# Kernel optimization log

Hardware: AMD Instinct MI355X
Metric: run time of the kernel (lower is better)

Reference implementation:

```python
import jax, jax.numpy as jnp
import numpy as np

NUM_TAGS = 64
SOS_IDX, EOS_IDX, PAD_IDX = 1, 2, 0
NEG = -10000.0


def _make_trans(key):
    t = np.array(jax.random.normal(key, (NUM_TAGS, NUM_TAGS), dtype=jnp.float32))
    t[SOS_IDX, :] = NEG
    t[:, EOS_IDX] = NEG
    t[:, PAD_IDX] = NEG
    t[PAD_IDX, :] = NEG
    t[PAD_IDX, EOS_IDX] = 0.0
    t[PAD_IDX, PAD_IDX] = 0.0
    return jnp.asarray(t)


def setup_inputs() -> dict:
    key = jax.random.key(0)
    k_h, k_len, k_tr = jax.random.split(key, 3)
    B, T = 256, 1024
    h = jax.random.normal(k_h, (B, T, NUM_TAGS), dtype=jnp.float32)
    # variable-length prefix mask (1.0 for valid steps)
    lengths = jax.random.randint(k_len, (B,), 1, T + 1)
    mask = (jnp.arange(T)[None, :] < lengths[:, None]).astype(jnp.float32)
    trans = _make_trans(k_tr)
    return {"h": h, "mask": mask, "trans": trans}


def reference(h, mask, trans):
    # h: [B, T, N] emissions; mask: [B, T]; trans: [N_next, N_prev]
    B, T, N = h.shape
    init = jnp.full((B, N), NEG, dtype=h.dtype).at[:, SOS_IDX].set(0.0)

    def step(score, xs):
        h_t, m_t = xs  # [B, N], [B]
        # score[b, prev] + emit[b, next] + trans[next, prev] -> lse over prev
        s = score[:, None, :] + h_t[:, :, None] + trans[None, :, :]
        new = jax.nn.logsumexp(s, axis=-1)  # [B, N]
        m = m_t[:, None]
        score = new * m + score * (1.0 - m)
        return score, None

    score, _ = jax.lax.scan(step, init, (jnp.swapaxes(h, 0, 1), mask.T))
    # terminal transition to EOS, then partition function per batch element
    return jax.nn.logsumexp(score + trans[EOS_IDX][None, :], axis=-1)  # [B]
```

## Files before the change

kernel.cpp:

```cpp
#include <hip/hip_runtime.h>

#define BATCH 256
#define TT 1024
#define NN 64
#define CHUNK 64
#define NCH (TT / CHUNK)
#define SOS 1
#define EOSI 2
#define LN2F 0.6931471805599453f
#define LOG2E 1.4426950408889634f

typedef short bf16x8 __attribute__((ext_vector_type(8)));
typedef float f32x4 __attribute__((ext_vector_type(4)));

__device__ __forceinline__ unsigned short f2bf(float x) {
  unsigned u = __float_as_uint(x);
  u += 0x7fffu + ((u >> 16) & 1u);
  return (unsigned short)(u >> 16);
}
__device__ __forceinline__ float bf2f(unsigned short v) { return __uint_as_float(((unsigned)v) << 16); }

__device__ __forceinline__ unsigned cvtpk(float lo, float hi) {
  unsigned r;
  asm("v_cvt_pk_bf16_f32 %0, %1, %2" : "=v"(r) : "v"(lo), "v"(hi));
  return r;
}

__device__ __forceinline__ int tadr(int k, int c) {
  return ((c >> 4) << 11) + ((k >> 5) << 10) + (((k >> 3) & 3) << 8) + ((c & 15) << 4) + ((k & 7) << 1);
}

__device__ __forceinline__ int wave_len(const float* mask, int b, int l) {
  float ls = 0.f;
#pragma unroll
  for (int c = 0; c < 4; ++c) {
    float4 m4 = *reinterpret_cast<const float4*>(mask + (size_t)b * TT + c * 256 + l * 4);
    ls += (m4.x + m4.y) + (m4.z + m4.w);
  }
#pragma unroll
  for (int m = 1; m < 64; m <<= 1) ls += __shfl_xor(ls, m, 64);
  return (int)(ls + 0.5f);
}

__global__ __launch_bounds__(64, 4) void crf_chunk(const float* __restrict__ h,
                                                   const float* __restrict__ mask,
                                                   const float* __restrict__ trans,
                                                   unsigned short* __restrict__ mats,
                                                   float* __restrict__ scales) {
  __shared__ char R[8192 + 256];
  float* ehs = (float*)(R + 8192);
  const int l = threadIdx.x;
  const int b = blockIdx.x & (BATCH - 1);
  const int c = blockIdx.x >> 8;

  const int len = wave_len(mask, b, l);
  const int t0 = c * CHUNK;
  if (t0 >= len) return;
  const int nstep = min(CHUNK, len - t0);

  bf16x8 ef[4][2];
#pragma unroll
  for (int I = 0; I < 4; ++I)
#pragma unroll
    for (int Kc = 0; Kc < 2; ++Kc) {
      const int row = 16 * I + (l & 15);
      const int k0 = 32 * Kc + 8 * (l >> 4);
      const float* p = trans + row * 64 + k0;
      bf16x8 v;
#pragma unroll
      for (int e = 0; e < 8; ++e) v[e] = (short)f2bf(__expf(p[e]));
      ef[I][Kc] = v;
    }

#pragma unroll
  for (int i = 0; i < 8; ++i) *(f32x4*)(R + ((i * 64 + l) << 4)) = f32x4{0.f, 0.f, 0.f, 0.f};
  *(unsigned short*)(R + tadr(l, l)) = 0x3F80;
  asm volatile("s_waitcnt lgkmcnt(0)" ::: "memory");

  int eA = 0, eB = 0, esum = 0;
  float hv = h[((size_t)b * TT + t0) * NN + l];

  for (int t = 0; t < nstep; ++t) {
    const int tn = (t + 1 < nstep) ? t + 1 : t;
    float hv_next = h[((size_t)b * TT + t0 + tn) * NN + l];
    ehs[l] = exp2f(fmaf(hv, LOG2E, (float)(-eA)));
    esum += eA;

    float mloc = 0.f;
#pragma unroll
    for (int J = 0; J < 4; ++J) {
      bf16x8 f0 = *(bf16x8*)(R + ((2 * J) << 10) + (l << 4));
      bf16x8 f1 = *(bf16x8*)(R + ((2 * J + 1) << 10) + (l << 4));
      f32x4 a[4];
#pragma unroll
      for (int I = 0; I < 4; ++I) a[I] = f32x4{0.f, 0.f, 0.f, 0.f};
#pragma unroll
      for (int I = 0; I < 4; ++I) {
        a[I] = __builtin_amdgcn_mfma_f32_16x16x32_bf16(ef[I][0], f0, a[I], 0, 0, 0);
        a[I] = __builtin_amdgcn_mfma_f32_16x16x32_bf16(ef[I][1], f1, a[I], 0, 0, 0);
      }
#pragma unroll
      for (int I = 0; I < 4; ++I) {
        f32x4 s4 = *(f32x4*)(ehs + 16 * I + 4 * (l >> 4));
        f32x4 v = a[I] * s4;
        mloc = fmaxf(mloc, fmaxf(fmaxf(v[0], v[1]), fmaxf(v[2], v[3])));
        const int r0 = 16 * I + 4 * (l >> 4);
        const int cc = 16 * J + (l & 15);
        *(uint2*)(R + tadr(r0, cc)) = uint2{cvtpk(v[0], v[1]), cvtpk(v[2], v[3])};
      }
    }
#pragma unroll
    for (int m = 1; m < 64; m <<= 1) mloc = fmaxf(mloc, __shfl_xor(mloc, m, 64));
    const int eNew = (__float_as_int(mloc) >> 23) - 127;
    eA = eB;
    eB = eNew;
    hv = hv_next;
    asm volatile("s_waitcnt lgkmcnt(0)" ::: "memory");
  }

  const float scF = __int_as_float((127 - eB) << 23);
  esum += eB;
  unsigned short* gm = mats + (size_t)(b * NCH + c) * 4096;
#pragma unroll
  for (int j0 = 0; j0 < 64; j0 += 8) {
    unsigned q[4];
#pragma unroll
    for (int p = 0; p < 4; ++p) {
      float x0 = bf2f(*(unsigned short*)(R + tadr(l, j0 + 2 * p))) * scF;
      float x1 = bf2f(*(unsigned short*)(R + tadr(l, j0 + 2 * p + 1))) * scF;
      q[p] = cvtpk(x0, x1);
    }
    *(uint4*)(gm + l * 64 + j0) = uint4{q[0], q[1], q[2], q[3]};
  }
  if (l == 0) scales[b * NCH + c] = LN2F * (float)esum;
}

__global__ __launch_bounds__(64) void crf_fold(const float* __restrict__ mask,
                                               const float* __restrict__ trans,
                                               const unsigned short* __restrict__ mats,
                                               const float* __restrict__ scales,
                                               float* __restrict__ out) {
  __shared__ float pv[NN];
  const int l = threadIdx.x;
  const int b = blockIdx.x;
  const int len = wave_len(mask, b, l);
  const int nc = (len + CHUNK - 1) / CHUNK;

  float stot = (l < nc) ? scales[b * NCH + l] : 0.f;
#pragma unroll
  for (int m = 1; m < 64; m <<= 1) stot += __shfl_xor(stot, m, 64);

  pv[l] = (l == SOS) ? 1.f : 0.f;
  asm volatile("s_waitcnt lgkmcnt(0)" ::: "memory");

  int eA = 0, esum = 0;
  for (int c = 0; c < nc; ++c) {
    const uint4* Mr = (const uint4*)(mats + (size_t)(b * NCH + c) * 4096 + l * 64);
    uint4 U[8];
#pragma unroll
    for (int j = 0; j < 8; ++j) U[j] = Mr[j];
    const float sc = __int_as_float((127 - eA) << 23);
    esum += eA;
    float ac0 = 0.f, ac1 = 0.f, ac2 = 0.f, ac3 = 0.f;
#pragma unroll
    for (int j = 0; j < 8; ++j) {
      f32x4 pa = *(f32x4*)(pv + j * 8);
      f32x4 pb = *(f32x4*)(pv + j * 8 + 4);
      uint4 q = U[j];
      ac0 = fmaf(__uint_as_float(q.x << 16), pa[0], ac0);
      ac1 = fmaf(__uint_as_float(q.x & 0xffff0000u), pa[1], ac1);
      ac2 = fmaf(__uint_as_float(q.y << 16), pa[2], ac2);
      ac3 = fmaf(__uint_as_float(q.y & 0xffff0000u), pa[3], ac3);
      ac0 = fmaf(__uint_as_float(q.z << 16), pb[0], ac0);
      ac1 = fmaf(__uint_as_float(q.z & 0xffff0000u), pb[1], ac1);
      ac2 = fmaf(__uint_as_float(q.w << 16), pb[2], ac2);
      ac3 = fmaf(__uint_as_float(q.w & 0xffff0000u), pb[3], ac3);
    }
    float pn = ((ac0 + ac1) + (ac2 + ac3)) * sc;
    float mm = pn;
#pragma unroll
    for (int m = 1; m < 64; m <<= 1) mm = fmaxf(mm, __shfl_xor(mm, m, 64));
    eA = (__float_as_int(mm) >> 23) - 127;
    pv[l] = pn;
    asm volatile("s_waitcnt lgkmcnt(0)" ::: "memory");
  }

  float s = pv[l] * __expf(trans[EOSI * NN + l]);
#pragma unroll
  for (int m = 1; m < 64; m <<= 1) s += __shfl_xor(s, m, 64);
  if (l == 0) out[b] = __logf(s) + LN2F * (float)esum + stot;
}

extern "C" void kernel_launch(void* const* d_in, const int* in_sizes, int n_in,
                              void* d_out, int out_size, void* d_ws, size_t ws_size,
                              hipStream_t stream) {
  const float* h = (const float*)d_in[0];
  const float* mask = (const float*)d_in[1];
  const float* trans = (const float*)d_in[2];
  float* out = (float*)d_out;

  unsigned short* mats = (unsigned short*)d_ws;
  float* scales = (float*)((char*)d_ws + (size_t)BATCH * NCH * 4096 * 2);

  hipLaunchKernelGGL(crf_chunk, dim3(BATCH * NCH), dim3(64), 0, stream, h, mask, trans, mats, scales);
  hipLaunchKernelGGL(crf_fold, dim3(BATCH), dim3(64), 0, stream, mask, trans, mats, scales, out);
}
```

Before: 179.2 us.

## Replace per-step wave max reduction with lagged single-lane exponent proxy

The per-step 64-lane shuffle max reduction that picks the rescaling exponent is replaced by one readlane of a proxy maximum. The proxy is taken from a subset of accumulator entries and applied only every other step, which removes a serial cross-lane dependency from the recurrence. The change also prefetches the next LDS B-fragments during the MFMA loop, uses packed f32 multiplies, loads emission scales once per step, remaps blocks to be batch-major, and lowers the occupancy hint. The risk is numerical: a single-entry proxy with a lagged rescale could let values drift toward bf16 overflow or underflow for atypical inputs.

```diff
diff --git a/kernel.cpp b/kernel.cpp
--- a/kernel.cpp
+++ b/kernel.cpp
@@ -12,6 +12,7 @@
 
 typedef short bf16x8 __attribute__((ext_vector_type(8)));
 typedef float f32x4 __attribute__((ext_vector_type(4)));
+typedef float f32x2 __attribute__((ext_vector_type(2)));
 
 __device__ __forceinline__ unsigned short f2bf(float x) {
   unsigned u = __float_as_uint(x);
@@ -25,6 +26,11 @@
   asm("v_cvt_pk_bf16_f32 %0, %1, %2" : "=v"(r) : "v"(lo), "v"(hi));
   return r;
 }
+__device__ __forceinline__ f32x2 pkmul(f32x2 a, f32x2 b) {
+  f32x2 r;
+  asm("v_pk_mul_f32 %0, %1, %2" : "=v"(r) : "v"(a), "v"(b));
+  return r;
+}
 
 __device__ __forceinline__ int tadr(int k, int c) {
   return ((c >> 4) << 11) + ((k >> 5) << 10) + (((k >> 3) & 3) << 8) + ((c & 15) << 4) + ((k & 7) << 1);
@@ -42,7 +48,7 @@
   return (int)(ls + 0.5f);
 }
 
-__global__ __launch_bounds__(64, 4) void crf_chunk(const float* __restrict__ h,
+__global__ __launch_bounds__(64, 3) void crf_chunk(const float* __restrict__ h,
                                                    const float* __restrict__ mask,
                                                    const float* __restrict__ trans,
                                                    unsigned short* __restrict__ mats,
@@ -50,8 +56,9 @@
   __shared__ char R[8192 + 256];
   float* ehs = (float*)(R + 8192);
   const int l = threadIdx.x;
-  const int b = blockIdx.x & (BATCH - 1);
-  const int c = blockIdx.x >> 8;
+  const int h4 = l >> 4;
+  const int b = blockIdx.x >> 4;
+  const int c = blockIdx.x & (NCH - 1);
 
   const int len = wave_len(mask, b, l);
   const int t0 = c * CHUNK;
@@ -64,8 +71,7 @@
 #pragma unroll
     for (int Kc = 0; Kc < 2; ++Kc) {
       const int row = 16 * I + (l & 15);
-      const int k0 = 32 * Kc + 8 * (l >> 4);
-      const float* p = trans + row * 64 + k0;
+      const float* p = trans + row * 64 + 32 * Kc + 8 * h4;
       bf16x8 v;
 #pragma unroll
       for (int e = 0; e < 8; ++e) v[e] = (short)f2bf(__expf(p[e]));
@@ -77,49 +83,65 @@
   *(unsigned short*)(R + tadr(l, l)) = 0x3F80;
   asm volatile("s_waitcnt lgkmcnt(0)" ::: "memory");
 
-  int eA = 0, eB = 0, esum = 0;
-  float hv = h[((size_t)b * TT + t0) * NN + l];
+  int ePend = 0;
+  int esum = 0;
+  const float* hp = h + ((size_t)b * TT + t0) * NN + l;
+  float hv = *hp;
+  hp += NN;
 
   for (int t = 0; t < nstep; ++t) {
-    const int tn = (t + 1 < nstep) ? t + 1 : t;
-    float hv_next = h[((size_t)b * TT + t0 + tn) * NN + l];
-    ehs[l] = exp2f(fmaf(hv, LOG2E, (float)(-eA)));
-    esum += eA;
-
-    float mloc = 0.f;
+    float hv_next = hv;
+    if (t + 1 < nstep) hv_next = *hp;
+    hp += NN;
+
+    const int ec = ((t & 1) == 0) ? ePend : 0;
+    esum += ec;
+    ehs[l] = exp2f(fmaf(hv, LOG2E, (float)(-ec)));
+    f32x4 eh4[4];
+#pragma unroll
+    for (int I = 0; I < 4; ++I) eh4[I] = *(f32x4*)(ehs + 16 * I + 4 * h4);
+
+    bf16x8 fc0 = *(bf16x8*)(R + 0 + (l << 4));
+    bf16x8 fc1 = *(bf16x8*)(R + 1024 + (l << 4));
+    float prox = 0.f;
 #pragma unroll
     for (int J = 0; J < 4; ++J) {
-      bf16x8 f0 = *(bf16x8*)(R + ((2 * J) << 10) + (l << 4));
-      bf16x8 f1 = *(bf16x8*)(R + ((2 * J + 1) << 10) + (l << 4));
+      bf16x8 fn0, fn1;
+      if (J < 3) {
+        fn0 = *(bf16x8*)(R + (2 * J + 2) * 1024 + (l << 4));
+        fn1 = *(bf16x8*)(R + (2 * J + 3) * 1024 + (l << 4));
+      }
       f32x4 a[4];
 #pragma unroll
       for (int I = 0; I < 4; ++I) a[I] = f32x4{0.f, 0.f, 0.f, 0.f};
 #pragma unroll
       for (int I = 0; I < 4; ++I) {
-        a[I] = __builtin_amdgcn_mfma_f32_16x16x32_bf16(ef[I][0], f0, a[I], 0, 0, 0);
-        a[I] = __builtin_amdgcn_mfma_f32_16x16x32_bf16(ef[I][1], f1, a[I], 0, 0, 0);
+        a[I] = __builtin_amdgcn_mfma_f32_16x16x32_bf16(ef[I][0], fc0, a[I], 0, 0, 0);
+        a[I] = __builtin_amdgcn_mfma_f32_16x16x32_bf16(ef[I][1], fc1, a[I], 0, 0, 0);
       }
 #pragma unroll
       for (int I = 0; I < 4; ++I) {
-        f32x4 s4 = *(f32x4*)(ehs + 16 * I + 4 * (l >> 4));
-        f32x4 v = a[I] * s4;
-        mloc = fmaxf(mloc, fmaxf(fmaxf(v[0], v[1]), fmaxf(v[2], v[3])));
-        const int r0 = 16 * I + 4 * (l >> 4);
+        f32x2 vlo = pkmul(f32x2{a[I][0], a[I][1]}, f32x2{eh4[I][0], eh4[I][1]});
+        f32x2 vhi = pkmul(f32x2{a[I][2], a[I][3]}, f32x2{eh4[I][2], eh4[I][3]});
+        if (J == 0 && (I == 1 || I == 2))
+          prox = fmaxf(prox, fmaxf(fmaxf(vlo[0], vlo[1]), fmaxf(vhi[0], vhi[1])));
+        const int r0 = 16 * I + 4 * h4;
         const int cc = 16 * J + (l & 15);
-        *(uint2*)(R + tadr(r0, cc)) = uint2{cvtpk(v[0], v[1]), cvtpk(v[2], v[3])};
+        *(uint2*)(R + tadr(r0, cc)) = uint2{cvtpk(vlo[0], vlo[1]), cvtpk(vhi[0], vhi[1])};
       }
-    }
-#pragma unroll
-    for (int m = 1; m < 64; m <<= 1) mloc = fmaxf(mloc, __shfl_xor(mloc, m, 64));
-    const int eNew = (__float_as_int(mloc) >> 23) - 127;
-    eA = eB;
-    eB = eNew;
+      fc0 = fn0;
+      fc1 = fn1;
+    }
+    if ((t & 1) == 0) {
+      float px = __int_as_float(__builtin_amdgcn_readlane(__float_as_int(prox), 5));
+      ePend = (__float_as_int(px) >> 23) - 127;
+    }
     hv = hv_next;
     asm volatile("s_waitcnt lgkmcnt(0)" ::: "memory");
   }
 
-  const float scF = __int_as_float((127 - eB) << 23);
-  esum += eB;
+  const float scF = __int_as_float((127 - ePend) << 23);
+  esum += ePend;
   unsigned short* gm = mats + (size_t)(b * NCH + c) * 4096;
 #pragma unroll
   for (int j0 = 0; j0 < 64; j0 += 8) {
```

New measurement: 146.0 us. -18.5%, faster.

## Split chunk transfer matrix across four waves with per-wave column slices and scales

Applied to the files above, without the earlier changes.

The chunk kernel now uses 256-thread blocks where each of four waves propagates a 16-column slice of the 64x64 chunk transfer matrix independently. This cuts each wave's per-step MFMA and LDS work by a factor of four and shortens the serial dependency chain. The emission exponentials are double-buffered and prefetched two steps ahead. The per-step max reduction shrinks to a partial shuffle plus readlane. Each wave keeps its own exponent, so the fold kernel rescales each 16-column group of the carried vector by the per-wave exponent differences. The cost is extra scale bookkeeping and a little more fold work, and the coarser rescaling carries some risk of range or precision loss.

```diff
diff --git a/kernel.cpp b/kernel.cpp
--- a/kernel.cpp
+++ b/kernel.cpp
@@ -4,7 +4,7 @@
 #define TT 1024
 #define NN 64
 #define CHUNK 64
-#define NCH (TT / CHUNK)
+#define NCH 16
 #define SOS 1
 #define EOSI 2
 #define LN2F 0.6931471805599453f
@@ -19,15 +19,14 @@
   return (unsigned short)(u >> 16);
 }
 __device__ __forceinline__ float bf2f(unsigned short v) { return __uint_as_float(((unsigned)v) << 16); }
-
 __device__ __forceinline__ unsigned cvtpk(float lo, float hi) {
   unsigned r;
   asm("v_cvt_pk_bf16_f32 %0, %1, %2" : "=v"(r) : "v"(lo), "v"(hi));
   return r;
 }
 
-__device__ __forceinline__ int tadr(int k, int c) {
-  return ((c >> 4) << 11) + ((k >> 5) << 10) + (((k >> 3) & 3) << 8) + ((c & 15) << 4) + ((k & 7) << 1);
+__device__ __forceinline__ int padr(int k, int c) {
+  return ((k >> 5) << 10) + (((k >> 3) & 3) << 8) + (c << 4) + ((k & 7) << 1);
 }
 
 __device__ __forceinline__ int wave_len(const float* mask, int b, int l) {
@@ -42,14 +41,21 @@
   return (int)(ls + 0.5f);
 }
 
-__global__ __launch_bounds__(64, 4) void crf_chunk(const float* __restrict__ h,
-                                                   const float* __restrict__ mask,
-                                                   const float* __restrict__ trans,
-                                                   unsigned short* __restrict__ mats,
-                                                   float* __restrict__ scales) {
-  __shared__ char R[8192 + 256];
-  float* ehs = (float*)(R + 8192);
-  const int l = threadIdx.x;
+__global__ __launch_bounds__(256, 4) void crf_chunk(const float* __restrict__ h,
+                                                    const float* __restrict__ mask,
+                                                    const float* __restrict__ trans,
+                                                    unsigned short* __restrict__ mats,
+                                                    int* __restrict__ scalesI) {
+  __shared__ char lds[4 * 2048 + 4 * 512];
+  const int tid = threadIdx.x;
+  const int w = tid >> 6;
+  const int l = tid & 63;
+  const int h4 = l >> 4;
+  const int cl = l & 15;
+  char* P = lds + w * 2048;
+  float* ehs0 = (float*)(lds + 8192 + w * 512);
+  float* ehs1 = ehs0 + 64;
+
   const int b = blockIdx.x & (BATCH - 1);
   const int c = blockIdx.x >> 8;
 
@@ -63,9 +69,7 @@
   for (int I = 0; I < 4; ++I)
 #pragma unroll
     for (int Kc = 0; Kc < 2; ++Kc) {
-      const int row = 16 * I + (l & 15);
-      const int k0 = 32 * Kc + 8 * (l >> 4);
-      const float* p = trans + row * 64 + k0;
+      const float* p = trans + (16 * I + cl) * 64 + 32 * Kc + 8 * h4;
       bf16x8 v;
 #pragma unroll
       for (int e = 0; e < 8; ++e) v[e] = (short)f2bf(__expf(p[e]));
@@ -73,72 +77,73 @@
     }
 
 #pragma unroll
-  for (int i = 0; i < 8; ++i) *(f32x4*)(R + ((i * 64 + l) << 4)) = f32x4{0.f, 0.f, 0.f, 0.f};
-  *(unsigned short*)(R + tadr(l, l)) = 0x3F80;
-  asm volatile("s_waitcnt lgkmcnt(0)" ::: "memory");
-
-  int eA = 0, eB = 0, esum = 0;
-  float hv = h[((size_t)b * TT + t0) * NN + l];
+  for (int i = 0; i < 2; ++i) *(f32x4*)(P + ((i * 64 + l) << 4)) = f32x4{0.f, 0.f, 0.f, 0.f};
+  if (l < 16) *(unsigned short*)(P + padr(16 * w + l, l)) = 0x3F80;
+
+  const float* hb = h + ((size_t)b * TT + t0) * NN + l;
+  ehs0[l] = exp2f(hb[0] * LOG2E);
+  asm volatile("" ::: "memory");
+
+  float hvN = hb[(size_t)min(1, nstep - 1) * NN];
+  float hvN2 = hb[(size_t)min(2, nstep - 1) * NN];
+  int esum = 0, ecCur = 0, eM1 = 0;
 
   for (int t = 0; t < nstep; ++t) {
-    const int tn = (t + 1 < nstep) ? t + 1 : t;
-    float hv_next = h[((size_t)b * TT + t0 + tn) * NN + l];
-    ehs[l] = exp2f(fmaf(hv, LOG2E, (float)(-eA)));
-    esum += eA;
-
-    float mloc = 0.f;
-#pragma unroll
-    for (int J = 0; J < 4; ++J) {
-      bf16x8 f0 = *(bf16x8*)(R + ((2 * J) << 10) + (l << 4));
-      bf16x8 f1 = *(bf16x8*)(R + ((2 * J + 1) << 10) + (l << 4));
-      f32x4 a[4];
-#pragma unroll
-      for (int I = 0; I < 4; ++I) a[I] = f32x4{0.f, 0.f, 0.f, 0.f};
-#pragma unroll
-      for (int I = 0; I < 4; ++I) {
-        a[I] = __builtin_amdgcn_mfma_f32_16x16x32_bf16(ef[I][0], f0, a[I], 0, 0, 0);
-        a[I] = __builtin_amdgcn_mfma_f32_16x16x32_bf16(ef[I][1], f1, a[I], 0, 0, 0);
-      }
-#pragma unroll
-      for (int I = 0; I < 4; ++I) {
-        f32x4 s4 = *(f32x4*)(ehs + 16 * I + 4 * (l >> 4));
-        f32x4 v = a[I] * s4;
-        mloc = fmaxf(mloc, fmaxf(fmaxf(v[0], v[1]), fmaxf(v[2], v[3])));
-        const int r0 = 16 * I + 4 * (l >> 4);
-        const int cc = 16 * J + (l & 15);
-        *(uint2*)(R + tadr(r0, cc)) = uint2{cvtpk(v[0], v[1]), cvtpk(v[2], v[3])};
-      }
-    }
-#pragma unroll
-    for (int m = 1; m < 64; m <<= 1) mloc = fmaxf(mloc, __shfl_xor(mloc, m, 64));
-    const int eNew = (__float_as_int(mloc) >> 23) - 127;
-    eA = eB;
-    eB = eNew;
-    hv = hv_next;
-    asm volatile("s_waitcnt lgkmcnt(0)" ::: "memory");
-  }
-
-  const float scF = __int_as_float((127 - eB) << 23);
-  esum += eB;
-  unsigned short* gm = mats + (size_t)(b * NCH + c) * 4096;
-#pragma unroll
-  for (int j0 = 0; j0 < 64; j0 += 8) {
-    unsigned q[4];
-#pragma unroll
-    for (int p = 0; p < 4; ++p) {
-      float x0 = bf2f(*(unsigned short*)(R + tadr(l, j0 + 2 * p))) * scF;
-      float x1 = bf2f(*(unsigned short*)(R + tadr(l, j0 + 2 * p + 1))) * scF;
-      q[p] = cvtpk(x0, x1);
-    }
-    *(uint4*)(gm + l * 64 + j0) = uint4{q[0], q[1], q[2], q[3]};
-  }
-  if (l == 0) scales[b * NCH + c] = LN2F * (float)esum;
+    esum += ecCur;
+    float* ehsW = ((t + 1) & 1) ? ehs1 : ehs0;
+    ehsW[l] = exp2f(fmaf(hvN, LOG2E, -(float)eM1));
+    ecCur = eM1;
+    hvN = hvN2;
+    hvN2 = hb[(size_t)min(t + 3, nstep - 1) * NN];
+
+    float* ehsR = (t & 1) ? ehs1 : ehs0;
+    bf16x8 fc0 = *(bf16x8*)(P + (l << 4));
+    bf16x8 fc1 = *(bf16x8*)(P + 1024 + (l << 4));
+    f32x4 eh4[4];
+#pragma unroll
+    for (int I = 0; I < 4; ++I) eh4[I] = *(f32x4*)(ehsR + 16 * I + 4 * h4);
+
+    f32x4 a[4];
+#pragma unroll
+    for (int I = 0; I < 4; ++I) a[I] = f32x4{0.f, 0.f, 0.f, 0.f};
+#pragma unroll
+    for (int I = 0; I < 4; ++I) {
+      a[I] = __builtin_amdgcn_mfma_f32_16x16x32_bf16(ef[I][0], fc0, a[I], 0, 0, 0);
+      a[I] = __builtin_amdgcn_mfma_f32_16x16x32_bf16(ef[I][1], fc1, a[I], 0, 0, 0);
+    }
+    float prox = 0.f;
+#pragma unroll
+    for (int I = 0; I < 4; ++I) {
+      f32x4 v = a[I] * eh4[I];
+      prox = fmaxf(prox, fmaxf(fmaxf(v[0], v[1]), fmaxf(v[2], v[3])));
+      *(uint2*)(P + padr(16 * I + 4 * h4, cl)) = uint2{cvtpk(v[0], v[1]), cvtpk(v[2], v[3])};
+    }
+    prox = fmaxf(prox, __shfl_xor(prox, 16, 64));
+    prox = fmaxf(prox, __shfl_xor(prox, 32, 64));
+    float px = __int_as_float(__builtin_amdgcn_readlane(__float_as_int(prox), 5));
+    eM1 = (__float_as_int(px) >> 23) - 127;
+    asm volatile("" ::: "memory");
+  }
+
+  const float scF = __int_as_float((127 - eM1) << 23);
+  esum += eM1;
+  unsigned short* gm = mats + (size_t)(b * NCH + c) * 4096 + l * 64 + 16 * w;
+  unsigned q[8];
+#pragma unroll
+  for (int p = 0; p < 8; ++p) {
+    float x0 = bf2f(*(unsigned short*)(P + padr(l, 2 * p))) * scF;
+    float x1 = bf2f(*(unsigned short*)(P + padr(l, 2 * p + 1))) * scF;
+    q[p] = cvtpk(x0, x1);
+  }
+  *(uint4*)gm = uint4{q[0], q[1], q[2], q[3]};
+  *(uint4*)(gm + 8) = uint4{q[4], q[5], q[6], q[7]};
+  if (l == 0) scalesI[(b * NCH + c) * 4 + w] = esum;
 }
 
 __global__ __launch_bounds__(64) void crf_fold(const float* __restrict__ mask,
                                                const float* __restrict__ trans,
                                                const unsigned short* __restrict__ mats,
-                                               const float* __restrict__ scales,
+                                               const int* __restrict__ scalesI,
                                                float* __restrict__ out) {
   __shared__ float pv[NN];
   const int l = threadIdx.x;
@@ -146,49 +151,52 @@
   const int len = wave_len(mask, b, l);
   const int nc = (len + CHUNK - 1) / CHUNK;
 
-  float stot = (l < nc) ? scales[b * NCH + l] : 0.f;
-#pragma unroll
-  for (int m = 1; m < 64; m <<= 1) stot += __shfl_xor(stot, m, 64);
-
-  pv[l] = (l == SOS) ? 1.f : 0.f;
-  asm volatile("s_waitcnt lgkmcnt(0)" ::: "memory");
-
-  int eA = 0, esum = 0;
+  float pr = (l == SOS) ? 1.f : 0.f;
+  int eA = 0;
+  long esumT = 0;
+
   for (int c = 0; c < nc; ++c) {
+    const int* sI = scalesI + (b * NCH + c) * 4;
+    const int e0 = sI[0], e1 = sI[1], e2 = sI[2], e3 = sI[3];
+    const int S = max(max(e0, e1), max(e2, e3));
+    const int g = l >> 4;
+    int dl = (g == 0) ? e0 : (g == 1) ? e1 : (g == 2) ? e2 : e3;
+    dl -= S;
+    pv[l] = ldexpf(pr, dl - eA);
+    asm volatile("" ::: "memory");
+    esumT += S + eA;
+
     const uint4* Mr = (const uint4*)(mats + (size_t)(b * NCH + c) * 4096 + l * 64);
     uint4 U[8];
 #pragma unroll
     for (int j = 0; j < 8; ++j) U[j] = Mr[j];
-    const float sc = __int_as_float((127 - eA) << 23);
-    esum += eA;
     float ac0 = 0.f, ac1 = 0.f, ac2 = 0.f, ac3 = 0.f;
 #pragma unroll
     for (int j = 0; j < 8; ++j) {
       f32x4 pa = *(f32x4*)(pv + j * 8);
       f32x4 pb = *(f32x4*)(pv + j * 8 + 4);
-      uint4 q = U[j];
-      ac0 = fmaf(__uint_as_float(q.x << 16), pa[0], ac0);
-      ac1 = fmaf(__uint_as_float(q.x & 0xffff0000u), pa[1], ac1);
-      ac2 = fmaf(__uint_as_float(q.y << 16), pa[2], ac2);
-      ac3 = fmaf(__uint_as_float(q.y & 0xffff0000u), pa[3], ac3);
-      ac0 = fmaf(__uint_as_float(q.z << 16), pb[0], ac0);
-      ac1 = fmaf(__uint_as_float(q.z & 0xffff0000u), pb[1], ac1);
-      ac2 = fmaf(__uint_as_float(q.w << 16), pb[2], ac2);
-      ac3 = fmaf(__uint_as_float(q.w & 0xffff0000u), pb[3], ac3);
-    }
-    float pn = ((ac0 + ac1) + (ac2 + ac3)) * sc;
-    float mm = pn;
+      uint4 qq = U[j];
+      ac0 = fmaf(__uint_as_float(qq.x << 16), pa[0], ac0);
+      ac1 = fmaf(__uint_as_float(qq.x & 0xffff0000u), pa[1], ac1);
+      ac2 = fmaf(__uint_as_float(qq.y << 16), pa[2], ac2);
+      ac3 = fmaf(__uint_as_float(qq.y & 0xffff0000u), pa[3], ac3);
+      ac0 = fmaf(__uint_as_float(qq.z << 16), pb[0], ac0);
+      ac1 = fmaf(__uint_as_float(qq.z & 0xffff0000u), pb[1], ac1);
+      ac2 = fmaf(__uint_as_float(qq.w << 16), pb[2], ac2);
+      ac3 = fmaf(__uint_as_float(qq.w & 0xffff0000u), pb[3], ac3);
+    }
+    pr = (ac0 + ac1) + (ac2 + ac3);
+    float mm = pr;
 #pragma unroll
     for (int m = 1; m < 64; m <<= 1) mm = fmaxf(mm, __shfl_xor(mm, m, 64));
     eA = (__float_as_int(mm) >> 23) - 127;
-    pv[l] = pn;
-    asm volatile("s_waitcnt lgkmcnt(0)" ::: "memory");
-  }
-
-  float s = pv[l] * __expf(trans[EOSI * NN + l]);
+    asm volatile("" ::: "memory");
+  }
+
+  float s = pr * __expf(trans[EOSI * NN + l]);
 #pragma unroll
   for (int m = 1; m < 64; m <<= 1) s += __shfl_xor(s, m, 64);
-  if (l == 0) out[b] = __logf(s) + LN2F * (float)esum + stot;
+  if (l == 0) out[b] = __logf(s) + LN2F * (float)esumT;
 }
 
 extern "C" void kernel_launch(void* const* d_in, const int* in_sizes, int n_in,
@@ -200,8 +208,8 @@
   float* out = (float*)d_out;
 
   unsigned short* mats = (unsigned short*)d_ws;
-  float* scales = (float*)((char*)d_ws + (size_t)BATCH * NCH * 4096 * 2);
-
-  hipLaunchKernelGGL(crf_chunk, dim3(BATCH * NCH), dim3(64), 0, stream, h, mask, trans, mats, scales);
-  hipLaunchKernelGGL(crf_fold, dim3(BATCH), dim3(64), 0, stream, mask, trans, mats, scales, out);
-}
+  int* scalesI = (int*)((char*)d_ws + (size_t)BATCH * NCH * 4096 * 2);
+
+  hipLaunchKernelGGL(crf_chunk, dim3(BATCH * NCH), dim3(256), 0, stream, h, mask, trans, mats, scalesI);
+  hipLaunchKernelGGL(crf_fold, dim3(BATCH), dim3(64), 0, stream, mask, trans, mats, scalesI, out);
+}
```

Result: faster. 154.7 us (-13.6%).
